# Performance work log

Measured on AMD Instinct MI355X. Metric: run time of the kernel, lower is better.

The kernel has to match this reference:

```python
import jax, jax.numpy as jnp
import numpy as np

B, S, D = 4, 2048, 2048
H = 16
DH = D // H  # 128

def _rope_tables(seq_len, d_head, base=10000.0):
    inv_freq = 1.0 / (base ** (np.arange(0, d_head, 2, dtype=np.float32) / d_head))
    pos = np.arange(seq_len, dtype=np.float32)
    ang = pos[:, None] * inv_freq[None, :]  # (S, d_head/2)
    return jnp.asarray(np.cos(ang)), jnp.asarray(np.sin(ang))

def setup_inputs() -> dict:
    key = jax.random.key(0)
    ks = jax.random.split(key, 4)
    x = jax.random.normal(ks[0], (B, S, D), dtype=jnp.float32)
    rope_cos, rope_sin = _rope_tables(S, DH)
    # Linear params, scaled like torch default init (~1/sqrt(fan_in))
    Wqkv = jax.random.normal(ks[1], (D, 3 * D), dtype=jnp.float32) / np.sqrt(D)
    bqkv = jnp.zeros((3 * D,), dtype=jnp.float32)
    Wout = jax.random.normal(ks[2], (D, D), dtype=jnp.float32) / np.sqrt(D)
    bout = jnp.zeros((D,), dtype=jnp.float32)
    return {"x": x, "rope_cos": rope_cos, "rope_sin": rope_sin,
            "Wqkv": Wqkv, "bqkv": bqkv, "Wout": Wout, "bout": bout}

def _apply_rope(x, cos, sin):
    # x: (B, H, S, DH); cos/sin: (S, DH/2), broadcast over B,H
    x1 = x[..., 0::2]
    x2 = x[..., 1::2]
    out = jnp.stack([x1 * cos - x2 * sin, x1 * sin + x2 * cos], axis=-1)
    return out.reshape(*out.shape[:-2], -1)  # interleave back to (..., DH)

def reference(x, rope_cos, rope_sin, Wqkv, bqkv, Wout, bout):
    qkv = (x @ Wqkv + bqkv).reshape(B, S, 3, H, DH)
    qkv = jnp.transpose(qkv, (2, 0, 3, 1, 4))  # (3, B, H, S, DH)
    q, k, v = qkv[0], qkv[1], qkv[2]
    q = _apply_rope(q, rope_cos, rope_sin)
    k = _apply_rope(k, rope_cos, rope_sin)
    scale = 1.0 / np.sqrt(DH)
    scores = jnp.einsum('bhqd,bhkd->bhqk', q, k) * scale  # (B,H,S,S)
    causal = jnp.tril(jnp.ones((S, S), dtype=bool))
    scores = jnp.where(causal, scores, jnp.finfo(scores.dtype).min)
    attn = jax.nn.softmax(scores, axis=-1)
    out = jnp.einsum('bhqk,bhkd->bhqd', attn, v)  # (B,H,S,DH)
    out = jnp.transpose(out, (0, 2, 1, 3)).reshape(B, S, D)
    return out @ Wout + bout
```

## Files before the change

### kernel.cpp

```cpp
#include <hip/hip_runtime.h>
#include <hip/hip_bf16.h>
#include <math.h>

typedef __attribute__((ext_vector_type(8))) short bf16x8;
typedef __attribute__((ext_vector_type(4))) float f32x4;
typedef __attribute__((ext_vector_type(16))) float f32x16;
typedef __attribute__((ext_vector_type(8))) unsigned short u16x8;
typedef __attribute__((ext_vector_type(4))) unsigned short u16x4;

static constexpr int B = 4, S = 2048, D = 2048, H = 16, DH = 128;
static constexpr int N3 = 3 * D;
static constexpr int M = B * S;

__device__ __forceinline__ unsigned short f2bf(float f) {
  unsigned u = __float_as_uint(f);
  u += 0x7fffu + ((u >> 16) & 1u);
  return (unsigned short)(u >> 16);
}
__device__ __forceinline__ float bf2f(unsigned short b) {
  return __uint_as_float(((unsigned)b) << 16);
}

__global__ __launch_bounds__(256) void cvt_kernel(const float* __restrict__ in,
                                                  unsigned short* __restrict__ out) {
  size_t i = (size_t)blockIdx.x * 256 + threadIdx.x;
  f32x4 v = *(const f32x4*)(in + i * 4);
  u16x4 o;
  o[0] = f2bf(v[0]); o[1] = f2bf(v[1]); o[2] = f2bf(v[2]); o[3] = f2bf(v[3]);
  *(u16x4*)(out + i * 4) = o;
}

__global__ __launch_bounds__(256) void transpose_kernel(const float* __restrict__ W,
                                                        unsigned short* __restrict__ WT,
                                                        int K, int N) {
  __shared__ float t[32][33];
  int tx = threadIdx.x, ty = threadIdx.y;
  int n0 = blockIdx.x * 32, k0 = blockIdx.y * 32;
#pragma unroll
  for (int i = 0; i < 4; i++)
    t[ty + i * 8][tx] = W[(size_t)(k0 + ty + i * 8) * N + n0 + tx];
  __syncthreads();
#pragma unroll
  for (int i = 0; i < 4; i++)
    WT[(size_t)(n0 + ty + i * 8) * K + k0 + tx] = f2bf(t[tx][ty + i * 8]);
}

__device__ __forceinline__ void gload_lds(const void* g, void* l) {
  __builtin_amdgcn_global_load_lds((const __attribute__((address_space(1))) void*)g,
                                   (__attribute__((address_space(3))) void*)l, 16, 0, 0);
}

template <int EPI>
__global__ __launch_bounds__(256) void gemm_bt(
    const unsigned short* __restrict__ A, const unsigned short* __restrict__ Bt,
    const float* __restrict__ bias, float* __restrict__ Cf,
    unsigned short* __restrict__ Qp, unsigned short* __restrict__ Kp,
    unsigned short* __restrict__ VTp, int Nn, int Kk) {
  __shared__ __align__(16) unsigned short lA[128 * 32];
  __shared__ __align__(16) unsigned short lB[128 * 32];
  const int tid = threadIdx.x;
  const int l = tid & 63;
  const int w = tid >> 6;
  const int lr = l >> 4, lc = l & 15;
  const int wr = w >> 1, wc = w & 1;
  const int bm = blockIdx.x, bn = blockIdx.y;

  f32x4 acc[4][4];
#pragma unroll
  for (int m = 0; m < 4; m++)
#pragma unroll
    for (int n = 0; n < 4; n++) acc[m][n] = (f32x4)0.f;

  const int srow = tid >> 2;
  const int sk = (tid & 3) * 8;
  const unsigned short* Ab = A + (size_t)(bm * 128 + srow) * Kk + sk;
  const unsigned short* Bb = Bt + (size_t)(bn * 128 + srow) * Kk + sk;
  unsigned short* lA0 = lA + (size_t)tid * 8;
  unsigned short* lB0 = lB + (size_t)tid * 8;

  for (int kt = 0; kt < Kk; kt += 32) {
    __syncthreads();
    gload_lds(Ab + kt, lA0);
    gload_lds(Ab + (size_t)64 * Kk + kt, lA0 + 256 * 8);
    gload_lds(Bb + kt, lB0);
    gload_lds(Bb + (size_t)64 * Kk + kt, lB0 + 256 * 8);
    __syncthreads();
    bf16x8 af[4], bfr[4];
#pragma unroll
    for (int m = 0; m < 4; m++)
      af[m] = *(const bf16x8*)(lA + (wr * 64 + m * 16 + lc) * 32 + lr * 8);
#pragma unroll
    for (int n = 0; n < 4; n++)
      bfr[n] = *(const bf16x8*)(lB + (wc * 64 + n * 16 + lc) * 32 + lr * 8);
#pragma unroll
    for (int m = 0; m < 4; m++)
#pragma unroll
      for (int n = 0; n < 4; n++)
        acc[m][n] = __builtin_amdgcn_mfma_f32_16x16x32_bf16(af[m], bfr[n], acc[m][n], 0, 0, 0);
  }

#pragma unroll
  for (int m = 0; m < 4; m++) {
#pragma unroll
    for (int n = 0; n < 4; n++) {
      const int col = bn * 128 + wc * 64 + n * 16 + lc;
      const float bv = bias[col];
#pragma unroll
      for (int r = 0; r < 4; r++) {
        const int row = bm * 128 + wr * 64 + m * 16 + lr * 4 + r;
        const float v = acc[m][n][r] + bv;
        if (EPI == 0) {
          const unsigned short ob = f2bf(v);
          const int b = row >> 11, s = row & 2047;
          const int which = col >> 11, within = col & 2047;
          const int h = within >> 7, d = within & 127;
          const size_t bh = (size_t)(b * H + h);
          if (which == 0)      Qp[(bh * S + s) * DH + d] = ob;
          else if (which == 1) Kp[(bh * S + s) * DH + d] = ob;
          else                 VTp[(bh * DH + d) * S + s] = ob;
        } else {
          Cf[(size_t)row * Nn + col] = v;
        }
      }
    }
  }
}

__global__ __launch_bounds__(256) void rope_kernel(unsigned short* __restrict__ T,
                                                   const float* __restrict__ cosT,
                                                   const float* __restrict__ sinT) {
  int t = blockIdx.x * 256 + threadIdx.x;
  int d8 = t & 15;
  int s = (t >> 4) & (S - 1);
  size_t off = (size_t)t * 8;
  u16x8 v = *(const u16x8*)(T + off);
  f32x4 c = *(const f32x4*)(cosT + (size_t)s * (DH / 2) + d8 * 4);
  f32x4 sn = *(const f32x4*)(sinT + (size_t)s * (DH / 2) + d8 * 4);
  u16x8 o;
#pragma unroll
  for (int j = 0; j < 4; j++) {
    float x1 = bf2f(v[2 * j]), x2 = bf2f(v[2 * j + 1]);
    o[2 * j]     = f2bf(x1 * c[j] - x2 * sn[j]);
    o[2 * j + 1] = f2bf(x1 * sn[j] + x2 * c[j]);
  }
  *(u16x8*)(T + off) = o;
}

__global__ __launch_bounds__(512, 1) void attn3_kernel(
    const unsigned short* __restrict__ Q, const unsigned short* __restrict__ Kt,
    const unsigned short* __restrict__ VT, unsigned short* __restrict__ O) {
  __shared__ __align__(16) unsigned short lK[2][32 * 128];
  __shared__ __align__(16) unsigned short lV[2][128 * 40];
  const int tid = threadIdx.x;
  const int w = tid >> 6;
  const int l = tid & 63;
  const int ql = l & 31;
  const int hi = l >> 5;
  const int j = blockIdx.x;
  const int bh = ((j >> 3) & 7) * 8 + (j & 7);
  const int pr = j >> 6;
  const int b = bh >> 4, h = bh & 15;
  const size_t base = (size_t)bh * S * DH;
  const float cl = 0.088388347648318447f * 1.44269504088896341f;

  const int kdst = (tid * 8) ^ (((tid >> 4) & 7) << 3);
  const unsigned short* Kgb = Kt + base;
  const int vdh = tid >> 2;
  const int vc = (tid & 3) * 8;
  const int vdst = vdh * 40 + vc;
  const unsigned short* Vgr = VT + ((size_t)bh * DH + vdh) * S;
  const int sfix = (ql & 7) << 3;

  for (int half = 0; half < 2; half++) {
    const int strip = half ? 7 - pr : pr;
    const int qw0 = strip * 256 + w * 32;

    bf16x8 qf[8];
    const unsigned short* qp = Q + base + (size_t)(qw0 + ql) * DH + hi * 8;
#pragma unroll
    for (int t = 0; t < 8; t++) qf[t] = *(const bf16x8*)(qp + t * 16);

    f32x16 acc[4];
#pragma unroll
    for (int mt = 0; mt < 4; mt++) acc[mt] = (f32x16)0.f;
    float m = -INFINITY, lsum = 0.f;

    const int ntb = 8 * (strip + 1);
    const int last = 8 * strip + w;

    {
      f32x4 kr = *(const f32x4*)(Kgb + tid * 8);
      f32x4 vr = *(const f32x4*)(Vgr + vc);
      *(f32x4*)(&lK[0][kdst]) = kr;
      *(f32x4*)(&lV[0][vdst]) = vr;
      __syncthreads();
    }

    for (int kb = 0; kb < ntb; kb++) {
      const int cur = kb & 1;
      const bool more = (kb + 1 < ntb);
      f32x4 kr, vr;
      if (more) {
        kr = *(const f32x4*)(Kgb + (size_t)(kb + 1) * 4096 + tid * 8);
        vr = *(const f32x4*)(Vgr + (kb + 1) * 32 + vc);
      }
      if (kb <= last) {
        const int kv0 = kb * 32;
        const unsigned short* kbuf = lK[cur];
        const unsigned short* vbuf = lV[cur];
        f32x16 st0 = (f32x16)0.f, st1 = (f32x16)0.f;
#pragma unroll
        for (int t = 0; t < 4; t++) {
          bf16x8 k0 = *(const bf16x8*)(kbuf + ((ql * 128 + (2 * t) * 16 + 8 * hi) ^ sfix));
          bf16x8 k1 = *(const bf16x8*)(kbuf + ((ql * 128 + (2 * t + 1) * 16 + 8 * hi) ^ sfix));
          st0 = __builtin_amdgcn_mfma_f32_32x32x16_bf16(k0, qf[2 * t], st0, 0, 0, 0);
          st1 = __builtin_amdgcn_mfma_f32_32x32x16_bf16(k1, qf[2 * t + 1], st1, 0, 0, 0);
        }
        float sv[16];
#pragma unroll
        for (int r = 0; r < 16; r++) sv[r] = st0[r] + st1[r];
        if (kb == last) {
#pragma unroll
          for (int r = 0; r < 16; r++) {
            const int klocal = (r & 3) + 8 * (r >> 2) + 4 * hi;
            sv[r] = (klocal > ql) ? -INFINITY : sv[r];
          }
        }
        float smax = sv[0];
#pragma unroll
        for (int r = 1; r < 16; r++) smax = fmaxf(smax, sv[r]);
        smax = fmaxf(smax, __shfl_xor(smax, 32));

        float fr = 1.f;
        if (!__all((smax - m) * cl <= 8.0f)) {
          const float mn = fmaxf(m, smax);
          fr = exp2f((m - mn) * cl);
          m = mn;
#pragma unroll
          for (int mt = 0; mt < 4; mt++)
#pragma unroll
            for (int r = 0; r < 16; r++) acc[mt][r] *= fr;
        }
        float p[16];
        float ps = 0.f;
#pragma unroll
        for (int r = 0; r < 16; r++) {
          p[r] = exp2f((sv[r] - m) * cl);
          ps += p[r];
        }
        lsum = lsum * fr + ps + __shfl_xor(ps, 32);

        unsigned W[8];
#pragma unroll
        for (int qd = 0; qd < 4; qd++) {
          W[2 * qd]     = (unsigned)f2bf(p[4 * qd])     | ((unsigned)f2bf(p[4 * qd + 1]) << 16);
          W[2 * qd + 1] = (unsigned)f2bf(p[4 * qd + 2]) | ((unsigned)f2bf(p[4 * qd + 3]) << 16);
        }
#pragma unroll
        for (int t = 0; t < 2; t++) {
          const unsigned s0 = hi ? W[4 * t] : W[4 * t + 2];
          const unsigned s1 = hi ? W[4 * t + 1] : W[4 * t + 3];
          const unsigned r0 = __shfl_xor((int)s0, 32);
          const unsigned r1 = __shfl_xor((int)s1, 32);
          union { unsigned u[4]; bf16x8 v; } pf;
          if (hi == 0) { pf.u[0] = W[4 * t]; pf.u[1] = W[4 * t + 1]; pf.u[2] = r0; pf.u[3] = r1; }
          else         { pf.u[0] = r0; pf.u[1] = r1; pf.u[2] = W[4 * t + 2]; pf.u[3] = W[4 * t + 3]; }
#pragma unroll
          for (int mt = 0; mt < 4; mt++) {
            const bf16x8 vf = *(const bf16x8*)(vbuf + (mt * 32 + ql) * 40 + 16 * t + 8 * hi);
            acc[mt] = __builtin_amdgcn_mfma_f32_32x32x16_bf16(vf, pf.v, acc[mt], 0, 0, 0);
          }
        }
        (void)kv0;
      }
      if (more) {
        *(f32x4*)(&lK[cur ^ 1][kdst]) = kr;
        *(f32x4*)(&lV[cur ^ 1][vdst]) = vr;
      }
      __syncthreads();
    }

    const float inv = 1.f / lsum;
    const int s_glob = qw0 + ql;
    unsigned short* op = O + ((size_t)(b * S + s_glob) * H + h) * DH;
#pragma unroll
    for (int mt = 0; mt < 4; mt++)
#pragma unroll
      for (int g = 0; g < 4; g++) {
        u16x4 ov;
#pragma unroll
        for (int jj = 0; jj < 4; jj++) ov[jj] = f2bf(acc[mt][4 * g + jj] * inv);
        *(u16x4*)(op + mt * 32 + 8 * g + 4 * hi) = ov;
      }
  }
}

extern "C" void kernel_launch(void* const* d_in, const int* in_sizes, int n_in,
                              void* d_out, int out_size, void* d_ws, size_t ws_size,
                              hipStream_t stream) {
  const float* x    = (const float*)d_in[0];
  const float* cosT = (const float*)d_in[1];
  const float* sinT = (const float*)d_in[2];
  const float* Wqkv = (const float*)d_in[3];
  const float* bqkv = (const float*)d_in[4];
  const float* Wout = (const float*)d_in[5];
  const float* bout = (const float*)d_in[6];

  char* ws = (char*)d_ws;
  unsigned short* xbf   = (unsigned short*)(ws);
  unsigned short* WqkvT = (unsigned short*)(ws + ((size_t)32 << 20));
  unsigned short* WoutT = (unsigned short*)(ws + ((size_t)56 << 20));
  unsigned short* VTb   = (unsigned short*)(ws + ((size_t)64 << 20));
  unsigned short* Qb = (unsigned short*)d_out;
  unsigned short* Kb = (unsigned short*)d_out + (size_t)M * D;
  unsigned short* Ob = xbf;

  cvt_kernel<<<M * D / 1024, 256, 0, stream>>>(x, xbf);
  transpose_kernel<<<dim3(N3 / 32, D / 32), dim3(32, 8), 0, stream>>>(Wqkv, WqkvT, D, N3);
  transpose_kernel<<<dim3(D / 32, D / 32), dim3(32, 8), 0, stream>>>(Wout, WoutT, D, D);
  gemm_bt<0><<<dim3(M / 128, N3 / 128), 256, 0, stream>>>(xbf, WqkvT, bqkv, nullptr,
                                                          Qb, Kb, VTb, N3, D);
  rope_kernel<<<(B * H * S * 16) / 256, 256, 0, stream>>>(Qb, cosT, sinT);
  rope_kernel<<<(B * H * S * 16) / 256, 256, 0, stream>>>(Kb, cosT, sinT);
  attn3_kernel<<<B * H * 4, 512, 0, stream>>>(Qb, Kb, VTb, Ob);
  gemm_bt<1><<<dim3(M / 128, D / 128), 256, 0, stream>>>(Ob, WoutT, bout, (float*)d_out,
                                                         nullptr, nullptr, nullptr, D, D);
}
```

Baseline: 580.8 us.

## Rewrite bf16 GEMM with 256x128 tiles, triple-buffered LDS pipeline and XCD swizzle

Restructures the GEMM kernel to use 512-thread blocks computing 256x128 tiles with a 64-wide K step, triple-buffered LDS staged through global_load_lds, and XOR-swizzled LDS layout to avoid bank conflicts. Loads for tile t+2 are issued while tile t is computed, with explicit vmcnt waits, barriers and raised priority around MFMA blocks. Block IDs are remapped so neighbouring tiles land on the same XCD for L2 reuse. Hardcodes K=2048 and larger LDS use (144KB), which limits occupancy to one block per CU.

```diff
diff --git a/kernel.cpp b/kernel.cpp
--- a/kernel.cpp
+++ b/kernel.cpp
@@ -51,19 +51,60 @@
 }
 
 template <int EPI>
-__global__ __launch_bounds__(256) void gemm_bt(
+__global__ __launch_bounds__(512, 1) void gemm_bt(
     const unsigned short* __restrict__ A, const unsigned short* __restrict__ Bt,
     const float* __restrict__ bias, float* __restrict__ Cf,
     unsigned short* __restrict__ Qp, unsigned short* __restrict__ Kp,
-    unsigned short* __restrict__ VTp, int Nn, int Kk) {
-  __shared__ __align__(16) unsigned short lA[128 * 32];
-  __shared__ __align__(16) unsigned short lB[128 * 32];
+    unsigned short* __restrict__ VTp, int Nn, int nbn) {
+  __shared__ __align__(16) unsigned short lds[3 * 24576];
+  constexpr int NT = 32;
   const int tid = threadIdx.x;
   const int l = tid & 63;
   const int w = tid >> 6;
   const int lr = l >> 4, lc = l & 15;
   const int wr = w >> 1, wc = w & 1;
-  const int bm = blockIdx.x, bn = blockIdx.y;
+
+  const int nwg = gridDim.x;
+  const int cpx = nwg >> 3;
+  const int wg = blockIdx.x;
+  const int swz = (wg & 7) * cpx + (wg >> 3);
+  const int bm = swz / nbn;
+  const int bn = swz - bm * nbn;
+
+  const unsigned short* As[4];
+  const unsigned short* Bs[2];
+  int ldA[4], ldB[2];
+#pragma unroll
+  for (int i = 0; i < 4; i++) {
+    const int g = i * 512 + tid;
+    const int r = g >> 3;
+    const int c8 = (g & 7) ^ (r & 7);
+    As[i] = A + (size_t)(bm * 256 + r) * 2048 + c8 * 8;
+    ldA[i] = g * 8;
+  }
+#pragma unroll
+  for (int i = 0; i < 2; i++) {
+    const int g = i * 512 + tid;
+    const int r = g >> 3;
+    const int c8 = (g & 7) ^ (r & 7);
+    Bs[i] = Bt + (size_t)(bn * 128 + r) * 2048 + c8 * 8;
+    ldB[i] = 16384 + g * 8;
+  }
+
+#define STAGE_HALF(t_, h_, bufb_)                              \
+  do {                                                         \
+    const int kt_ = (t_) * 64;                                 \
+    unsigned short* ub_ = lds + (bufb_) * 24576;               \
+    if ((h_) == 0) {                                           \
+      gload_lds(As[0] + kt_, ub_ + ldA[0]);                    \
+      gload_lds(As[1] + kt_, ub_ + ldA[1]);                    \
+      gload_lds(Bs[0] + kt_, ub_ + ldB[0]);                    \
+    } else {                                                   \
+      gload_lds(As[2] + kt_, ub_ + ldA[2]);                    \
+      gload_lds(As[3] + kt_, ub_ + ldA[3]);                    \
+      gload_lds(Bs[1] + kt_, ub_ + ldB[1]);                    \
+    }                                                          \
+  } while (0)
 
   f32x4 acc[4][4];
 #pragma unroll
@@ -71,33 +112,52 @@
 #pragma unroll
     for (int n = 0; n < 4; n++) acc[m][n] = (f32x4)0.f;
 
-  const int srow = tid >> 2;
-  const int sk = (tid & 3) * 8;
-  const unsigned short* Ab = A + (size_t)(bm * 128 + srow) * Kk + sk;
-  const unsigned short* Bb = Bt + (size_t)(bn * 128 + srow) * Kk + sk;
-  unsigned short* lA0 = lA + (size_t)tid * 8;
-  unsigned short* lB0 = lB + (size_t)tid * 8;
-
-  for (int kt = 0; kt < Kk; kt += 32) {
-    __syncthreads();
-    gload_lds(Ab + kt, lA0);
-    gload_lds(Ab + (size_t)64 * Kk + kt, lA0 + 256 * 8);
-    gload_lds(Bb + kt, lB0);
-    gload_lds(Bb + (size_t)64 * Kk + kt, lB0 + 256 * 8);
-    __syncthreads();
-    bf16x8 af[4], bfr[4];
-#pragma unroll
-    for (int m = 0; m < 4; m++)
-      af[m] = *(const bf16x8*)(lA + (wr * 64 + m * 16 + lc) * 32 + lr * 8);
-#pragma unroll
-    for (int n = 0; n < 4; n++)
-      bfr[n] = *(const bf16x8*)(lB + (wc * 64 + n * 16 + lc) * 32 + lr * 8);
-#pragma unroll
-    for (int m = 0; m < 4; m++)
+  STAGE_HALF(0, 0, 0); STAGE_HALF(0, 1, 0);
+  STAGE_HALF(1, 0, 1); STAGE_HALF(1, 1, 1);
+  __builtin_amdgcn_sched_barrier(0);
+  asm volatile("s_waitcnt vmcnt(6)" ::: "memory");
+  __builtin_amdgcn_s_barrier();
+  __builtin_amdgcn_sched_barrier(0);
+
+  int cur = 0;
+  for (int t = 0; t < NT; t++) {
+    const int s2 = (cur >= 1) ? cur - 1 : cur + 2;
+    unsigned short* buf = lds + cur * 24576;
+    const bool stg = (t + 2) < NT;
+#pragma unroll
+    for (int kh = 0; kh < 2; kh++) {
+      const int ko = (kh * 32 + lr * 8) ^ ((lc & 7) << 3);
+      bf16x8 af[4], bfr[4];
+#pragma unroll
+      for (int m = 0; m < 4; m++)
+        af[m] = *(const bf16x8*)(buf + (wr * 64 + m * 16 + lc) * 64 + ko);
 #pragma unroll
       for (int n = 0; n < 4; n++)
-        acc[m][n] = __builtin_amdgcn_mfma_f32_16x16x32_bf16(af[m], bfr[n], acc[m][n], 0, 0, 0);
-  }
+        bfr[n] = *(const bf16x8*)(buf + 16384 + (wc * 64 + n * 16 + lc) * 64 + ko);
+      if (stg) STAGE_HALF(t + 2, kh, s2);
+      __builtin_amdgcn_sched_barrier(0);
+      __builtin_amdgcn_s_barrier();
+      asm volatile("s_waitcnt lgkmcnt(0)" ::: "memory");
+      __builtin_amdgcn_sched_barrier(0);
+      __builtin_amdgcn_s_setprio(1);
+#pragma unroll
+      for (int m = 0; m < 4; m++)
+#pragma unroll
+        for (int n = 0; n < 4; n++)
+          acc[m][n] = __builtin_amdgcn_mfma_f32_16x16x32_bf16(af[m], bfr[n], acc[m][n], 0, 0, 0);
+      __builtin_amdgcn_s_setprio(0);
+      __builtin_amdgcn_sched_barrier(0);
+      if (kh == 1) {
+        if (stg) asm volatile("s_waitcnt vmcnt(6)" ::: "memory");
+        else     asm volatile("s_waitcnt vmcnt(0)" ::: "memory");
+        __builtin_amdgcn_sched_barrier(0);
+      }
+      __builtin_amdgcn_s_barrier();
+      __builtin_amdgcn_sched_barrier(0);
+    }
+    cur = (cur == 2) ? 0 : cur + 1;
+  }
+#undef STAGE_HALF
 
 #pragma unroll
   for (int m = 0; m < 4; m++) {
@@ -107,7 +167,7 @@
       const float bv = bias[col];
 #pragma unroll
       for (int r = 0; r < 4; r++) {
-        const int row = bm * 128 + wr * 64 + m * 16 + lr * 4 + r;
+        const int row = bm * 256 + wr * 64 + m * 16 + lr * 4 + r;
         const float v = acc[m][n][r] + bv;
         if (EPI == 0) {
           const unsigned short ob = f2bf(v);
@@ -205,7 +265,6 @@
         vr = *(const f32x4*)(Vgr + (kb + 1) * 32 + vc);
       }
       if (kb <= last) {
-        const int kv0 = kb * 32;
         const unsigned short* kbuf = lK[cur];
         const unsigned short* vbuf = lV[cur];
         f32x16 st0 = (f32x16)0.f, st1 = (f32x16)0.f;
@@ -271,7 +330,6 @@
             acc[mt] = __builtin_amdgcn_mfma_f32_32x32x16_bf16(vf, pf.v, acc[mt], 0, 0, 0);
           }
         }
-        (void)kv0;
       }
       if (more) {
         *(f32x4*)(&lK[cur ^ 1][kdst]) = kr;
@@ -318,11 +376,11 @@
   cvt_kernel<<<M * D / 1024, 256, 0, stream>>>(x, xbf);
   transpose_kernel<<<dim3(N3 / 32, D / 32), dim3(32, 8), 0, stream>>>(Wqkv, WqkvT, D, N3);
   transpose_kernel<<<dim3(D / 32, D / 32), dim3(32, 8), 0, stream>>>(Wout, WoutT, D, D);
-  gemm_bt<0><<<dim3(M / 128, N3 / 128), 256, 0, stream>>>(xbf, WqkvT, bqkv, nullptr,
-                                                          Qb, Kb, VTb, N3, D);
+  gemm_bt<0><<<dim3((M / 256) * (N3 / 128)), 512, 0, stream>>>(xbf, WqkvT, bqkv, nullptr,
+                                                               Qb, Kb, VTb, N3, N3 / 128);
   rope_kernel<<<(B * H * S * 16) / 256, 256, 0, stream>>>(Qb, cosT, sinT);
   rope_kernel<<<(B * H * S * 16) / 256, 256, 0, stream>>>(Kb, cosT, sinT);
   attn3_kernel<<<B * H * 4, 512, 0, stream>>>(Qb, Kb, VTb, Ob);
-  gemm_bt<1><<<dim3(M / 128, D / 128), 256, 0, stream>>>(Ob, WoutT, bout, (float*)d_out,
-                                                         nullptr, nullptr, nullptr, D, D);
-}
+  gemm_bt<1><<<dim3((M / 256) * (D / 128)), 512, 0, stream>>>(Ob, WoutT, bout, (float*)d_out,
+                                                              nullptr, nullptr, nullptr, D, D / 128);
+}
```

Result: faster. 528.1 us (-9.1%).

## Rewrite GEMM as 256x256-tile, 4-stage pipelined 512-thread kernel with swizzled LDS

Applied to the files above, without the earlier changes.

Replaces the simple 128x128 single-buffered bf16 GEMM with a 256x256 tile per 512-thread workgroup. It stages K-tiles through a 4-deep LDS ring using direct global-to-LDS loads, with explicit vmcnt waits and barriers so loads overlap the MFMA work. It also XOR-swizzles the LDS layout to avoid bank conflicts, remaps the 1D grid in chunks of 8 for cache locality, and raises MFMA wave priority. The costs are hardcoding K=2048 and large LDS use (128KB, one workgroup per CU), with fragile hand-written wait counts.

```diff
diff --git a/kernel.cpp b/kernel.cpp
--- a/kernel.cpp
+++ b/kernel.cpp
@@ -51,63 +51,120 @@
 }
 
 template <int EPI>
-__global__ __launch_bounds__(256) void gemm_bt(
+__global__ __launch_bounds__(512, 1) void gemm_bt(
     const unsigned short* __restrict__ A, const unsigned short* __restrict__ Bt,
     const float* __restrict__ bias, float* __restrict__ Cf,
     unsigned short* __restrict__ Qp, unsigned short* __restrict__ Kp,
-    unsigned short* __restrict__ VTp, int Nn, int Kk) {
-  __shared__ __align__(16) unsigned short lA[128 * 32];
-  __shared__ __align__(16) unsigned short lB[128 * 32];
+    unsigned short* __restrict__ VTp, int Nn, int nbn) {
+  __shared__ __align__(16) unsigned short lds[4 * 16384];
+  constexpr int NT = 64;
   const int tid = threadIdx.x;
   const int l = tid & 63;
   const int w = tid >> 6;
   const int lr = l >> 4, lc = l & 15;
-  const int wr = w >> 1, wc = w & 1;
-  const int bm = blockIdx.x, bn = blockIdx.y;
-
-  f32x4 acc[4][4];
-#pragma unroll
-  for (int m = 0; m < 4; m++)
+  const int wm = w >> 2, wn = w & 3;
+
+  const int nwg = gridDim.x;
+  const int cpx = nwg >> 3;
+  const int wg = blockIdx.x;
+  const int swz = (wg & 7) * cpx + (wg >> 3);
+  const int bm = swz / nbn;
+  const int bn = swz - bm * nbn;
+
+  const unsigned short* Asrc[2];
+  const unsigned short* Bsrc[2];
+  int ldA[2], ldB[2];
+#pragma unroll
+  for (int i = 0; i < 2; i++) {
+    const int gi = i * 512 + tid;
+    const int r = gi >> 2, c = gi & 3;
+    const int cs = c ^ ((r >> 1) & 3);
+    Asrc[i] = A + (size_t)(bm * 256 + r) * 2048 + cs * 8;
+    ldA[i] = gi * 8;
+    Bsrc[i] = Bt + (size_t)(bn * 256 + r) * 2048 + cs * 8;
+    ldB[i] = 8192 + gi * 8;
+  }
+
+  f32x4 acc[8][4];
+#pragma unroll
+  for (int m = 0; m < 8; m++)
 #pragma unroll
     for (int n = 0; n < 4; n++) acc[m][n] = (f32x4)0.f;
 
-  const int srow = tid >> 2;
-  const int sk = (tid & 3) * 8;
-  const unsigned short* Ab = A + (size_t)(bm * 128 + srow) * Kk + sk;
-  const unsigned short* Bb = Bt + (size_t)(bn * 128 + srow) * Kk + sk;
-  unsigned short* lA0 = lA + (size_t)tid * 8;
-  unsigned short* lB0 = lB + (size_t)tid * 8;
-
-  for (int kt = 0; kt < Kk; kt += 32) {
-    __syncthreads();
-    gload_lds(Ab + kt, lA0);
-    gload_lds(Ab + (size_t)64 * Kk + kt, lA0 + 256 * 8);
-    gload_lds(Bb + kt, lB0);
-    gload_lds(Bb + (size_t)64 * Kk + kt, lB0 + 256 * 8);
-    __syncthreads();
-    bf16x8 af[4], bfr[4];
+  const int swzr = (lr ^ ((lc >> 1) & 3)) * 8;
+  const int aoff = (wm * 128 + lc) * 32 + swzr;
+  const int boff = 8192 + (wn * 64 + lc) * 32 + swzr;
+
+#pragma unroll
+  for (int t = 0; t < 3; t++) {
+    unsigned short* sb = lds + t * 16384;
+    gload_lds(Asrc[0] + t * 32, sb + ldA[0]);
+    gload_lds(Asrc[1] + t * 32, sb + ldA[1]);
+    gload_lds(Bsrc[0] + t * 32, sb + ldB[0]);
+    gload_lds(Bsrc[1] + t * 32, sb + ldB[1]);
+  }
+  __builtin_amdgcn_sched_barrier(0);
+  asm volatile("s_waitcnt vmcnt(8)" ::: "memory");
+  __builtin_amdgcn_s_barrier();
+  __builtin_amdgcn_sched_barrier(0);
+
+  for (int kt = 0; kt < NT; kt++) {
+    const unsigned short* buf = lds + (kt & 3) * 16384;
+    unsigned short* sb = lds + ((kt + 3) & 3) * 16384;
+    const bool stg = (kt + 3) < NT;
+    const int ks = (kt + 3) * 32;
+    bf16x8 a0[4], bb[4];
+#pragma unroll
+    for (int mf = 0; mf < 4; mf++) a0[mf] = *(const bf16x8*)(buf + aoff + mf * 512);
+#pragma unroll
+    for (int nf = 0; nf < 4; nf++) bb[nf] = *(const bf16x8*)(buf + boff + nf * 512);
+    if (stg) { gload_lds(Asrc[0] + ks, sb + ldA[0]); gload_lds(Asrc[1] + ks, sb + ldA[1]); }
+    __builtin_amdgcn_sched_barrier(0);
+    __builtin_amdgcn_s_barrier();
+    asm volatile("s_waitcnt lgkmcnt(0)" ::: "memory");
+    __builtin_amdgcn_sched_barrier(0);
+    __builtin_amdgcn_s_setprio(1);
 #pragma unroll
     for (int m = 0; m < 4; m++)
-      af[m] = *(const bf16x8*)(lA + (wr * 64 + m * 16 + lc) * 32 + lr * 8);
-#pragma unroll
-    for (int n = 0; n < 4; n++)
-      bfr[n] = *(const bf16x8*)(lB + (wc * 64 + n * 16 + lc) * 32 + lr * 8);
+#pragma unroll
+      for (int n = 0; n < 4; n++)
+        acc[m][n] = __builtin_amdgcn_mfma_f32_16x16x32_bf16(a0[m], bb[n], acc[m][n], 0, 0, 0);
+    __builtin_amdgcn_s_setprio(0);
+    __builtin_amdgcn_sched_barrier(0);
+    __builtin_amdgcn_s_barrier();
+    bf16x8 a1[4];
+#pragma unroll
+    for (int mf = 0; mf < 4; mf++) a1[mf] = *(const bf16x8*)(buf + aoff + (mf + 4) * 512);
+    if (stg) { gload_lds(Bsrc[0] + ks, sb + ldB[0]); gload_lds(Bsrc[1] + ks, sb + ldB[1]); }
+    __builtin_amdgcn_sched_barrier(0);
+    __builtin_amdgcn_s_barrier();
+    asm volatile("s_waitcnt lgkmcnt(0)" ::: "memory");
+    __builtin_amdgcn_sched_barrier(0);
+    __builtin_amdgcn_s_setprio(1);
 #pragma unroll
     for (int m = 0; m < 4; m++)
 #pragma unroll
       for (int n = 0; n < 4; n++)
-        acc[m][n] = __builtin_amdgcn_mfma_f32_16x16x32_bf16(af[m], bfr[n], acc[m][n], 0, 0, 0);
-  }
-
-#pragma unroll
-  for (int m = 0; m < 4; m++) {
+        acc[m + 4][n] = __builtin_amdgcn_mfma_f32_16x16x32_bf16(a1[m], bb[n], acc[m + 4][n], 0, 0, 0);
+    __builtin_amdgcn_s_setprio(0);
+    __builtin_amdgcn_sched_barrier(0);
+    if (kt + 3 < NT)      asm volatile("s_waitcnt vmcnt(8)" ::: "memory");
+    else if (kt + 2 < NT) asm volatile("s_waitcnt vmcnt(4)" ::: "memory");
+    else if (kt + 1 < NT) asm volatile("s_waitcnt vmcnt(0)" ::: "memory");
+    __builtin_amdgcn_sched_barrier(0);
+    __builtin_amdgcn_s_barrier();
+    __builtin_amdgcn_sched_barrier(0);
+  }
+
+#pragma unroll
+  for (int m = 0; m < 8; m++) {
 #pragma unroll
     for (int n = 0; n < 4; n++) {
-      const int col = bn * 128 + wc * 64 + n * 16 + lc;
+      const int col = bn * 256 + wn * 64 + n * 16 + lc;
       const float bv = bias[col];
 #pragma unroll
       for (int r = 0; r < 4; r++) {
-        const int row = bm * 128 + wr * 64 + m * 16 + lr * 4 + r;
+        const int row = bm * 256 + wm * 128 + m * 16 + lr * 4 + r;
         const float v = acc[m][n][r] + bv;
         if (EPI == 0) {
           const unsigned short ob = f2bf(v);
@@ -205,7 +262,6 @@
         vr = *(const f32x4*)(Vgr + (kb + 1) * 32 + vc);
       }
       if (kb <= last) {
-        const int kv0 = kb * 32;
         const unsigned short* kbuf = lK[cur];
         const unsigned short* vbuf = lV[cur];
         f32x16 st0 = (f32x16)0.f, st1 = (f32x16)0.f;
@@ -271,7 +327,6 @@
             acc[mt] = __builtin_amdgcn_mfma_f32_32x32x16_bf16(vf, pf.v, acc[mt], 0, 0, 0);
           }
         }
-        (void)kv0;
       }
       if (more) {
         *(f32x4*)(&lK[cur ^ 1][kdst]) = kr;
@@ -318,11 +373,11 @@
   cvt_kernel<<<M * D / 1024, 256, 0, stream>>>(x, xbf);
   transpose_kernel<<<dim3(N3 / 32, D / 32), dim3(32, 8), 0, stream>>>(Wqkv, WqkvT, D, N3);
   transpose_kernel<<<dim3(D / 32, D / 32), dim3(32, 8), 0, stream>>>(Wout, WoutT, D, D);
-  gemm_bt<0><<<dim3(M / 128, N3 / 128), 256, 0, stream>>>(xbf, WqkvT, bqkv, nullptr,
-                                                          Qb, Kb, VTb, N3, D);
+  gemm_bt<0><<<dim3((M / 256) * (N3 / 256)), 512, 0, stream>>>(xbf, WqkvT, bqkv, nullptr,
+                                                               Qb, Kb, VTb, N3, N3 / 256);
   rope_kernel<<<(B * H * S * 16) / 256, 256, 0, stream>>>(Qb, cosT, sinT);
   rope_kernel<<<(B * H * S * 16) / 256, 256, 0, stream>>>(Kb, cosT, sinT);
   attn3_kernel<<<B * H * 4, 512, 0, stream>>>(Qb, Kb, VTb, Ob);
-  gemm_bt<1><<<dim3(M / 128, D / 128), 256, 0, stream>>>(Ob, WoutT, bout, (float*)d_out,
-                                                         nullptr, nullptr, nullptr, D, D);
-}
+  gemm_bt<1><<<dim3((M / 256) * (D / 256)), 512, 0, stream>>>(Ob, WoutT, bout, (float*)d_out,
+                                                              nullptr, nullptr, nullptr, D, D / 256);
+}
```

Measured after the change: 502.2 us. -13.5%, faster.

## Rewrite bf16 GEMM with 256x256 tiles, double-buffered LDS pipeline and XCD swizzle

Applied to the files above, without the earlier changes.

Replaces the 128x128 single-buffer GEMM with a 512-thread, 256x256-tile kernel. It uses a double-buffered 128KB LDS pipeline that issues global-to-LDS loads for the next K tile while MFMAs run on the current one, and XOR-swizzles the LDS layout to avoid bank conflicts. It adds manual waitcnt/barrier scheduling, setprio around MFMA bursts, and a 1D grid remapped so neighbouring tiles land on the same XCD for L2 reuse. The aim is to cut load stalls and barrier overhead in the QKV and output projections. The risks are lower occupancy (one block per CU), hardcoded K=2048, and grid counts that must stay divisible by 8.

```diff
diff --git a/kernel.cpp b/kernel.cpp
--- a/kernel.cpp
+++ b/kernel.cpp
@@ -51,63 +51,122 @@
 }
 
 template <int EPI>
-__global__ __launch_bounds__(256) void gemm_bt(
+__global__ __launch_bounds__(512, 1) void gemm_bt(
     const unsigned short* __restrict__ A, const unsigned short* __restrict__ Bt,
     const float* __restrict__ bias, float* __restrict__ Cf,
     unsigned short* __restrict__ Qp, unsigned short* __restrict__ Kp,
-    unsigned short* __restrict__ VTp, int Nn, int Kk) {
-  __shared__ __align__(16) unsigned short lA[128 * 32];
-  __shared__ __align__(16) unsigned short lB[128 * 32];
+    unsigned short* __restrict__ VTp, int Nn, int nbn) {
+  __shared__ __align__(16) unsigned short lds[65536];
+  constexpr int NT = 32;
   const int tid = threadIdx.x;
   const int l = tid & 63;
   const int w = tid >> 6;
-  const int lr = l >> 4, lc = l & 15;
-  const int wr = w >> 1, wc = w & 1;
-  const int bm = blockIdx.x, bn = blockIdx.y;
-
-  f32x4 acc[4][4];
-#pragma unroll
-  for (int m = 0; m < 4; m++)
+  const int lc = l & 15, lr = l >> 4;
+  const int wm = w >> 2, wn = w & 3;
+
+  const int nwg = gridDim.x;
+  const int cpx = nwg >> 3;
+  const int wg = blockIdx.x;
+  const int swz = (wg & 7) * cpx + (wg >> 3);
+  const int bm = swz / nbn;
+  const int bn = swz - bm * nbn;
+
+  const int lq = l >> 2, lg = l & 3;
+  const int gsw = lg ^ ((l >> 3) & 3);
+  const unsigned short* sA[2];
+  const unsigned short* sB[2];
+  int dA[2], dB[2];
+#pragma unroll
+  for (int mh = 0; mh < 2; mh++) {
+    const int rowA = mh * 64 + wn * 16 + lq;
+    sA[mh] = A + (size_t)(bm * 256 + wm * 128 + rowA) * 2048 + gsw * 8;
+    dA[mh] = wm * 8192 + rowA * 32 + lg * 8;
+    const int rowB = (wm * 2 + (wn & 1)) * 32 + mh * 16 + lq;
+    sB[mh] = Bt + (size_t)(bn * 256 + (wn >> 1) * 128 + rowB) * 2048 + gsw * 8;
+    dB[mh] = 32768 + (wn >> 1) * 8192 + rowB * 32 + lg * 8;
+  }
+
+  const int rsw = (lr ^ ((lc >> 1) & 3)) * 8;
+  const int frA = wm * 8192 + lc * 32 + rsw;
+  const int frB = 32768 + (wn >> 1) * 8192 + ((wn & 1) * 64 + lc) * 32 + rsw;
+
+  f32x4 acc[8][4];
+#pragma unroll
+  for (int m = 0; m < 8; m++)
 #pragma unroll
     for (int n = 0; n < 4; n++) acc[m][n] = (f32x4)0.f;
 
-  const int srow = tid >> 2;
-  const int sk = (tid & 3) * 8;
-  const unsigned short* Ab = A + (size_t)(bm * 128 + srow) * Kk + sk;
-  const unsigned short* Bb = Bt + (size_t)(bn * 128 + srow) * Kk + sk;
-  unsigned short* lA0 = lA + (size_t)tid * 8;
-  unsigned short* lB0 = lB + (size_t)tid * 8;
-
-  for (int kt = 0; kt < Kk; kt += 32) {
-    __syncthreads();
-    gload_lds(Ab + kt, lA0);
-    gload_lds(Ab + (size_t)64 * Kk + kt, lA0 + 256 * 8);
-    gload_lds(Bb + kt, lB0);
-    gload_lds(Bb + (size_t)64 * Kk + kt, lB0 + 256 * 8);
-    __syncthreads();
-    bf16x8 af[4], bfr[4];
-#pragma unroll
-    for (int m = 0; m < 4; m++)
-      af[m] = *(const bf16x8*)(lA + (wr * 64 + m * 16 + lc) * 32 + lr * 8);
-#pragma unroll
-    for (int n = 0; n < 4; n++)
-      bfr[n] = *(const bf16x8*)(lB + (wc * 64 + n * 16 + lc) * 32 + lr * 8);
-#pragma unroll
-    for (int m = 0; m < 4; m++)
-#pragma unroll
-      for (int n = 0; n < 4; n++)
-        acc[m][n] = __builtin_amdgcn_mfma_f32_16x16x32_bf16(af[m], bfr[n], acc[m][n], 0, 0, 0);
-  }
-
-#pragma unroll
-  for (int m = 0; m < 4; m++) {
+#define STG(t1, kh, mh)                                                          \
+  do {                                                                           \
+    const int dbo_ = ((t1) & 1) * 16384 + (kh) * 4096;                           \
+    const int ko_ = (t1) * 64 + (kh) * 32;                                       \
+    gload_lds(sA[mh] + ko_, lds + dbo_ + dA[mh]);                                \
+    gload_lds(sB[mh] + ko_, lds + dbo_ + dB[mh]);                                \
+  } while (0)
+
+  STG(0, 0, 0); STG(0, 0, 1); STG(0, 1, 0); STG(0, 1, 1);
+  __builtin_amdgcn_sched_barrier(0);
+  asm volatile("s_waitcnt vmcnt(0)" ::: "memory");
+  __builtin_amdgcn_s_barrier();
+  __builtin_amdgcn_sched_barrier(0);
+
+  bf16x8 bfr[4];
+
+#define PHASE(db, kh, mh, DOSTG, t1)                                             \
+  do {                                                                           \
+    bf16x8 af0, af1, af2, af3;                                                   \
+    const int ab_ = (db) * 16384 + (kh) * 4096 + frA + (mh) * 2048;              \
+    af0 = *(const bf16x8*)(lds + ab_);                                           \
+    af1 = *(const bf16x8*)(lds + ab_ + 512);                                     \
+    af2 = *(const bf16x8*)(lds + ab_ + 1024);                                    \
+    af3 = *(const bf16x8*)(lds + ab_ + 1536);                                    \
+    if (mh == 0) {                                                               \
+      const int bb_ = (db) * 16384 + (kh) * 4096 + frB;                          \
+      bfr[0] = *(const bf16x8*)(lds + bb_);                                      \
+      bfr[1] = *(const bf16x8*)(lds + bb_ + 512);                                \
+      bfr[2] = *(const bf16x8*)(lds + bb_ + 1024);                               \
+      bfr[3] = *(const bf16x8*)(lds + bb_ + 1536);                               \
+    }                                                                            \
+    if (DOSTG) STG(t1, kh, mh);                                                  \
+    __builtin_amdgcn_sched_barrier(0);                                           \
+    asm volatile("s_waitcnt lgkmcnt(0)" ::: "memory");                           \
+    __builtin_amdgcn_sched_barrier(0);                                           \
+    __builtin_amdgcn_s_setprio(1);                                               \
+    _Pragma("unroll")                                                            \
+    for (int nt = 0; nt < 4; nt++) {                                             \
+      acc[(mh)*4 + 0][nt] = __builtin_amdgcn_mfma_f32_16x16x32_bf16(af0, bfr[nt], acc[(mh)*4 + 0][nt], 0, 0, 0); \
+      acc[(mh)*4 + 1][nt] = __builtin_amdgcn_mfma_f32_16x16x32_bf16(af1, bfr[nt], acc[(mh)*4 + 1][nt], 0, 0, 0); \
+      acc[(mh)*4 + 2][nt] = __builtin_amdgcn_mfma_f32_16x16x32_bf16(af2, bfr[nt], acc[(mh)*4 + 2][nt], 0, 0, 0); \
+      acc[(mh)*4 + 3][nt] = __builtin_amdgcn_mfma_f32_16x16x32_bf16(af3, bfr[nt], acc[(mh)*4 + 3][nt], 0, 0, 0); \
+    }                                                                            \
+    __builtin_amdgcn_s_setprio(0);                                               \
+    __builtin_amdgcn_sched_barrier(0);                                           \
+    asm volatile("s_waitcnt vmcnt(4)" ::: "memory");                             \
+    __builtin_amdgcn_s_barrier();                                                \
+    __builtin_amdgcn_sched_barrier(0);                                           \
+  } while (0)
+
+#pragma unroll 2
+  for (int t = 0; t < NT; t++) {
+    const int db = t & 1;
+    const bool dg = (t + 1) < NT;
+    PHASE(db, 0, 0, dg, t + 1);
+    PHASE(db, 0, 1, dg, t + 1);
+    PHASE(db, 1, 0, dg, t + 1);
+    PHASE(db, 1, 1, dg, t + 1);
+  }
+#undef PHASE
+#undef STG
+
+#pragma unroll
+  for (int m = 0; m < 8; m++) {
 #pragma unroll
     for (int n = 0; n < 4; n++) {
-      const int col = bn * 128 + wc * 64 + n * 16 + lc;
+      const int col = bn * 256 + wn * 64 + n * 16 + lc;
       const float bv = bias[col];
 #pragma unroll
       for (int r = 0; r < 4; r++) {
-        const int row = bm * 128 + wr * 64 + m * 16 + lr * 4 + r;
+        const int row = bm * 256 + wm * 128 + (m >> 2) * 64 + (m & 3) * 16 + lr * 4 + r;
         const float v = acc[m][n][r] + bv;
         if (EPI == 0) {
           const unsigned short ob = f2bf(v);
@@ -205,7 +264,6 @@
         vr = *(const f32x4*)(Vgr + (kb + 1) * 32 + vc);
       }
       if (kb <= last) {
-        const int kv0 = kb * 32;
         const unsigned short* kbuf = lK[cur];
         const unsigned short* vbuf = lV[cur];
         f32x16 st0 = (f32x16)0.f, st1 = (f32x16)0.f;
@@ -271,7 +329,6 @@
             acc[mt] = __builtin_amdgcn_mfma_f32_32x32x16_bf16(vf, pf.v, acc[mt], 0, 0, 0);
           }
         }
-        (void)kv0;
       }
       if (more) {
         *(f32x4*)(&lK[cur ^ 1][kdst]) = kr;
@@ -318,11 +375,11 @@
   cvt_kernel<<<M * D / 1024, 256, 0, stream>>>(x, xbf);
   transpose_kernel<<<dim3(N3 / 32, D / 32), dim3(32, 8), 0, stream>>>(Wqkv, WqkvT, D, N3);
   transpose_kernel<<<dim3(D / 32, D / 32), dim3(32, 8), 0, stream>>>(Wout, WoutT, D, D);
-  gemm_bt<0><<<dim3(M / 128, N3 / 128), 256, 0, stream>>>(xbf, WqkvT, bqkv, nullptr,
-                                                          Qb, Kb, VTb, N3, D);
+  gemm_bt<0><<<dim3((M / 256) * (N3 / 256)), 512, 0, stream>>>(xbf, WqkvT, bqkv, nullptr,
+                                                               Qb, Kb, VTb, N3, N3 / 256);
   rope_kernel<<<(B * H * S * 16) / 256, 256, 0, stream>>>(Qb, cosT, sinT);
   rope_kernel<<<(B * H * S * 16) / 256, 256, 0, stream>>>(Kb, cosT, sinT);
   attn3_kernel<<<B * H * 4, 512, 0, stream>>>(Qb, Kb, VTb, Ob);
-  gemm_bt<1><<<dim3(M / 128, D / 128), 256, 0, stream>>>(Ob, WoutT, bout, (float*)d_out,
-                                                         nullptr, nullptr, nullptr, D, D);
-}
+  gemm_bt<1><<<dim3((M / 256) * (D / 256)), 512, 0, stream>>>(Ob, WoutT, bout, (float*)d_out,
+                                                              nullptr, nullptr, nullptr, D, D / 256);
+}
```

Result: faster. 487.0 us (-16.2%).
